# Kernel tuning notes

Measured on AMD Instinct MI355X. Metric: run time of the kernel, lower is better.

## Reference

```python
import jax, jax.numpy as jnp
import numpy as np

N_T = 100  # number of time grid points for the ODE solve, matching torch.linspace(0, 1, 100)


def setup_inputs() -> dict:
    key = jax.random.key(0)
    kx, kw, kb, kc, kd = jax.random.split(key, 5)
    H = 1024
    N = 16384
    return {
        "x": jax.random.normal(kx, (N, H), dtype=jnp.float32),
        "W": jax.random.normal(kw, (H, H), dtype=jnp.float32),
        "b": jax.random.normal(kb, (H,), dtype=jnp.float32),
        "c": jax.random.normal(kc, (H,), dtype=jnp.float32),
        "d": jax.random.normal(kd, (H,), dtype=jnp.float32),
    }


def reference(x, W, b, c, d):
    # fused matmul + trig elementwise: z = x @ W + b*sin(x) + c*cos(x) + d*tan(x)
    z = jnp.matmul(x, W) + b * jnp.sin(x) + c * jnp.cos(x) + d * jnp.tan(x)

    # ODE: dy/dt = -y + t*z, y(0)=0, integrated on linspace(0,1,100), return y(1).
    ts = jnp.linspace(0.0, 1.0, N_T, dtype=z.dtype)
    t0 = ts[:-1]
    dts = ts[1:] - ts[:-1]

    def f(t, y):
        return -y + t * z

    def rk4_step(y, t_dt):
        t, dt = t_dt
        k1 = f(t, y)
        k2 = f(t + 0.5 * dt, y + 0.5 * dt * k1)
        k3 = f(t + 0.5 * dt, y + 0.5 * dt * k2)
        k4 = f(t + dt, y + dt * k3)
        y_next = y + (dt / 6.0) * (k1 + 2.0 * k2 + 2.0 * k3 + k4)
        return y_next, None

    y0 = jnp.zeros_like(z)
    y_final, _ = jax.lax.scan(rk4_step, y0, (t0, dts))
    return y_final
```

## Files before the change

### kernel.cpp

```cpp
#include <hip/hip_runtime.h>
#include <hip/hip_bf16.h>

typedef __attribute__((ext_vector_type(4))) float  f32x4;
typedef __attribute__((ext_vector_type(8))) short  bf16x8;
typedef __attribute__((ext_vector_type(4))) short  bf16x4v;

#define BM 128
#define BN 128
#define BK 64
#define PADK 72
#define EPAD 68
#define SMEM_BYTES 36864

__device__ __forceinline__ unsigned short f2bf(float f) {
  __hip_bfloat16 h = __float2bfloat16(f);
  unsigned short u; __builtin_memcpy(&u, &h, 2); return u;
}
__device__ __forceinline__ float bf2f(short u) {
  unsigned int w = ((unsigned int)(unsigned short)u) << 16;
  float f; __builtin_memcpy(&f, &w, 4); return f;
}

__device__ __forceinline__ void my_sincos(float xf, float& s_out, float& c_out) {
  const float kf = __builtin_rintf(xf * 0.636619772367581343f);
  const int   q  = (int)kf;
  const double kd = (double)kf;
  double rd = __builtin_fma(-kd, 1.5707963267948966,    (double)xf);
  rd        = __builtin_fma(-kd, 6.123233995736766e-17, rd);
  const float r = (float)rd;
  const float z = r * r;
  const float ps = fmaf(z, fmaf(z, fmaf(z, 2.7183114939898219e-06f,
                                           -1.9839334836096632e-04f),
                                   8.3333293858894632e-03f),
                        -1.6666666641626524e-01f);
  const float sr = fmaf(r * z, ps, r);
  const float pc = fmaf(z, fmaf(z, fmaf(z, 2.4390448796277409e-05f,
                                           -1.3886763774609929e-03f),
                                   4.1666623323739063e-02f),
                        -4.9999999725103100e-01f);
  const float cr = fmaf(z, pc, 1.0f);
  const bool swap = (q & 1) != 0;
  float s1 = swap ? cr : sr;
  float c1 = swap ? sr : cr;
  if (q & 2)       s1 = -s1;
  if ((q + 1) & 2) c1 = -c1;
  s_out = s1; c_out = c1;
}

__global__ __launch_bounds__(256)
void prep_all(const float* __restrict__ W, const float* __restrict__ x,
              const float* __restrict__ bv, const float* __restrict__ cv,
              const float* __restrict__ dv,
              unsigned short* __restrict__ Wt, unsigned short* __restrict__ xb,
              unsigned short* __restrict__ g, int H, int n4) {
  __shared__ float tile[64][65];
  const int t = threadIdx.x;
  if (blockIdx.x < 256) {
    const int blk = blockIdx.x;
    const int n0 = (blk & 15) << 6;
    const int k0 = (blk >> 4) << 6;
    #pragma unroll
    for (int it = 0; it < 4; ++it) {
      int q = it * 256 + t;
      int r = q >> 4, c4 = (q & 15) << 2;
      f32x4 v = *(const f32x4*)&W[(size_t)(k0 + r) * H + n0 + c4];
      tile[r][c4 + 0] = v[0]; tile[r][c4 + 1] = v[1];
      tile[r][c4 + 2] = v[2]; tile[r][c4 + 3] = v[3];
    }
    __syncthreads();
    #pragma unroll
    for (int it = 0; it < 4; ++it) {
      int q = it * 256 + t;
      int r = q >> 4, c4 = (q & 15) << 2;
      bf16x4v o;
      #pragma unroll
      for (int j = 0; j < 4; ++j) o[j] = (short)f2bf(tile[c4 + j][r]);
      *(bf16x4v*)&Wt[(size_t)(n0 + r) * H + k0 + c4] = o;
    }
  } else {
    const int jm = (H >> 2) - 1;
    int i = (blockIdx.x - 256) * 256 + t;
    const int stride = ((int)gridDim.x - 256) * 256;
    for (; i < n4; i += stride) {
      f32x4 v = ((const f32x4*)x)[i];
      const int j4 = (i & jm) << 2;
      f32x4 b4 = *(const f32x4*)&bv[j4];
      f32x4 c4 = *(const f32x4*)&cv[j4];
      f32x4 d4 = *(const f32x4*)&dv[j4];
      bf16x4v xo, go;
      #pragma unroll
      for (int e = 0; e < 4; ++e) {
        xo[e] = (short)f2bf(v[e]);
        float s, co;
        my_sincos(v[e], s, co);
        const float tn = s * __builtin_amdgcn_rcpf(co);
        go[e] = (short)f2bf(fmaf(b4[e], s, fmaf(c4[e], co, d4[e] * tn)));
      }
      ((bf16x4v*)xb)[i] = xo;
      ((bf16x4v*)g)[i]  = go;
    }
  }
}

__global__ __launch_bounds__(256)
void transpose_W(const float* __restrict__ W, unsigned short* __restrict__ Wt, int H) {
  __shared__ float tile[64][65];
  const int k0 = blockIdx.y * 64;
  const int n0 = blockIdx.x * 64;
  const int t = threadIdx.x;
  #pragma unroll
  for (int it = 0; it < 4; ++it) {
    int q = it * 256 + t;
    int r = q >> 4, c4 = (q & 15) << 2;
    f32x4 v = *(const f32x4*)&W[(size_t)(k0 + r) * H + n0 + c4];
    tile[r][c4 + 0] = v[0]; tile[r][c4 + 1] = v[1];
    tile[r][c4 + 2] = v[2]; tile[r][c4 + 3] = v[3];
  }
  __syncthreads();
  #pragma unroll
  for (int it = 0; it < 4; ++it) {
    int q = it * 256 + t;
    int r = q >> 4, c4 = (q & 15) << 2;
    bf16x4v o;
    #pragma unroll
    for (int j = 0; j < 4; ++j) o[j] = (short)f2bf(tile[c4 + j][r]);
    *(bf16x4v*)&Wt[(size_t)(n0 + r) * H + k0 + c4] = o;
  }
}
__global__ __launch_bounds__(256)
void cvt_x(const float* __restrict__ x, unsigned short* __restrict__ xb, int n4) {
  int i = blockIdx.x * 256 + threadIdx.x;
  const int stride = gridDim.x * 256;
  for (; i < n4; i += stride) {
    f32x4 v = ((const f32x4*)x)[i];
    bf16x4v o;
    #pragma unroll
    for (int j = 0; j < 4; ++j) o[j] = (short)f2bf(v[j]);
    ((bf16x4v*)xb)[i] = o;
  }
}

template <int MODE>
__global__ __launch_bounds__(256, 2)
void gemm_fused(const float* __restrict__ x, const unsigned short* __restrict__ xb,
                const unsigned short* __restrict__ Wt,
                const unsigned short* __restrict__ g,
                const float* __restrict__ bv, const float* __restrict__ cv,
                const float* __restrict__ dv, float* __restrict__ out,
                float S, int H) {
  __shared__ unsigned char smem[SMEM_BYTES];
  unsigned short* As = (unsigned short*)smem;
  unsigned short* Bs = As + BM * PADK;
  float*          Es = (float*)smem;

  const int tid  = threadIdx.x;
  const int nwg  = gridDim.x;
  const int work = (blockIdx.x & 7) * (nwg >> 3) + (blockIdx.x >> 3);
  const int bj   = work & 7;
  const int bi   = work >> 3;
  const int i0   = bi * BM, j0 = bj * BN;
  const int wave = tid >> 6, lane = tid & 63;
  const int wr = wave >> 1, wc = wave & 1;
  const int l16 = lane & 15, lq = lane >> 4;

  f32x4 acc[4][4] = {};

  for (int kk = 0; kk < H; kk += BK) {
    if constexpr (MODE <= 1) {
      #pragma unroll
      for (int it = 0; it < 4; ++it) {
        int q = it * 256 + tid;
        int r = q >> 3, c8 = (q & 7) << 3;
        bf16x8 v = *(const bf16x8*)&xb[(size_t)(i0 + r) * H + kk + c8];
        *(bf16x8*)&As[r * PADK + c8] = v;
      }
    } else {
      #pragma unroll
      for (int it = 0; it < 8; ++it) {
        int q = it * 256 + tid;
        int r = q >> 4, c4 = (q & 15) << 2;
        f32x4 v = *(const f32x4*)&x[(size_t)(i0 + r) * H + kk + c4];
        bf16x4v o;
        #pragma unroll
        for (int j = 0; j < 4; ++j) o[j] = (short)f2bf(v[j]);
        *(bf16x4v*)&As[r * PADK + c4] = o;
      }
    }
    #pragma unroll
    for (int it = 0; it < 4; ++it) {
      int q = it * 256 + tid;
      int r = q >> 3, c8 = (q & 7) << 3;
      bf16x8 v = *(const bf16x8*)&Wt[(size_t)(j0 + r) * H + kk + c8];
      *(bf16x8*)&Bs[r * PADK + c8] = v;
    }
    __syncthreads();

    #pragma unroll
    for (int s = 0; s < 2; ++s) {
      bf16x8 af[4], bfr[4];
      #pragma unroll
      for (int mi = 0; mi < 4; ++mi)
        af[mi] = *(const bf16x8*)&As[(wr * 64 + mi * 16 + l16) * PADK + s * 32 + lq * 8];
      #pragma unroll
      for (int ni = 0; ni < 4; ++ni)
        bfr[ni] = *(const bf16x8*)&Bs[(wc * 64 + ni * 16 + l16) * PADK + s * 32 + lq * 8];
      #pragma unroll
      for (int mi = 0; mi < 4; ++mi)
        #pragma unroll
        for (int ni = 0; ni < 4; ++ni)
          acc[mi][ni] = __builtin_amdgcn_mfma_f32_16x16x32_bf16(af[mi], bfr[ni], acc[mi][ni], 0, 0, 0);
    }
    __syncthreads();
  }

  float* ep = Es + wave * (16 * EPAD);
  const int rr = lane >> 2;
  const int cq = (lane & 3) * 16;
  #pragma unroll
  for (int mi = 0; mi < 4; ++mi) {
    #pragma unroll
    for (int ni = 0; ni < 4; ++ni)
      #pragma unroll
      for (int r = 0; r < 4; ++r)
        ep[(lq * 4 + r) * EPAD + ni * 16 + l16] = acc[mi][ni][r];
    const int i  = i0 + wr * 64 + mi * 16 + rr;
    const int jb = j0 + wc * 64 + cq;
    float* orow = &out[(size_t)i * H + jb];
    if constexpr (MODE == 0) {
      const unsigned short* grow = &g[(size_t)i * H + jb];
      #pragma unroll
      for (int t = 0; t < 4; ++t) {
        f32x4 a = *(const f32x4*)&ep[rr * EPAD + cq + 4 * t];
        bf16x4v gv = *(const bf16x4v*)&grow[4 * t];
        f32x4 o;
        #pragma unroll
        for (int e = 0; e < 4; ++e) o[e] = S * (a[e] + bf2f(gv[e]));
        *(f32x4*)&orow[4 * t] = o;
      }
    } else {
      const float* xrow = &x[(size_t)i * H + jb];
      #pragma unroll
      for (int t = 0; t < 4; ++t) {
        f32x4 a  = *(const f32x4*)&ep[rr * EPAD + cq + 4 * t];
        f32x4 xv = *(const f32x4*)&xrow[4 * t];
        f32x4 b4 = *(const f32x4*)&bv[jb + 4 * t];
        f32x4 c4 = *(const f32x4*)&cv[jb + 4 * t];
        f32x4 d4 = *(const f32x4*)&dv[jb + 4 * t];
        f32x4 o;
        #pragma unroll
        for (int e = 0; e < 4; ++e) {
          float s, co;
          my_sincos(xv[e], s, co);
          const float tanv = s * __builtin_amdgcn_rcpf(co);
          o[e] = S * (fmaf(b4[e], s, a[e]) + fmaf(c4[e], co, d4[e] * tanv));
        }
        *(f32x4*)&orow[4 * t] = o;
      }
    }
  }
}

extern "C" void kernel_launch(void* const* d_in, const int* in_sizes, int n_in,
                              void* d_out, int out_size, void* d_ws, size_t ws_size,
                              hipStream_t stream) {
  const float* x = (const float*)d_in[0];
  const float* W = (const float*)d_in[1];
  const float* b = (const float*)d_in[2];
  const float* c = (const float*)d_in[3];
  const float* d = (const float*)d_in[4];
  float* out = (float*)d_out;
  const int H = in_sizes[2];
  const int M = in_sizes[0] / H;

  const int NT = 100;
  float ts[NT];
  const float step = (float)(1.0 / 99.0);
  for (int i = 0; i < NT; ++i) ts[i] = (float)i * step;
  ts[NT - 1] = 1.0f;
  double yy = 0.0;
  for (int i = 0; i < NT - 1; ++i) {
    const double t = (double)ts[i], dt = (double)(ts[i + 1] - ts[i]);
    const double k1 = t - yy;
    const double k2 = (t + 0.5 * dt) - (yy + 0.5 * dt * k1);
    const double k3 = (t + 0.5 * dt) - (yy + 0.5 * dt * k2);
    const double k4 = (t + dt) - (yy + dt * k3);
    yy += dt / 6.0 * (k1 + 2.0 * k2 + 2.0 * k3 + k4);
  }
  const float S = (float)yy;

  unsigned short* Wt = (unsigned short*)d_ws;
  unsigned short* xb = Wt + (size_t)H * H;
  unsigned short* g  = xb + (size_t)M * H;
  const size_t needW  = (size_t)H * H * 2;
  const size_t needXb = (size_t)M * H * 2;
  const int n4   = M * H / 4;
  const int nblk = (H / BN) * (M / BM);

  if (ws_size >= needW + 2 * needXb) {
    prep_all<<<256 + 2048, 256, 0, stream>>>(W, x, b, c, d, Wt, xb, g, H, n4);
    gemm_fused<0><<<nblk, 256, 0, stream>>>(x, xb, Wt, g, b, c, d, out, S, H);
  } else if (ws_size >= needW + needXb) {
    dim3 tgrid(H / 64, H / 64);
    transpose_W<<<tgrid, 256, 0, stream>>>(W, Wt, H);
    cvt_x<<<2048, 256, 0, stream>>>(x, xb, n4);
    gemm_fused<1><<<nblk, 256, 0, stream>>>(x, xb, Wt, nullptr, b, c, d, out, S, H);
  } else {
    dim3 tgrid(H / 64, H / 64);
    transpose_W<<<tgrid, 256, 0, stream>>>(W, Wt, H);
    gemm_fused<2><<<nblk, 256, 0, stream>>>(x, nullptr, Wt, nullptr, b, c, d, out, S, H);
  }
}
```

Measured before the change: 85.92 us.

## Double-buffer GEMM K-loop with direct global-to-LDS loads in MODE 0

For MODE 0, the GEMM main loop now uses __builtin_amdgcn_global_load_lds to stream bf16 A and B tiles straight into LDS. The tiles are double-buffered with BK=32 so the next tile's load overlaps the current MFMA work, and there is one barrier per step. This removes the register round-trip for tile staging and the second barrier per iteration. The tiles use an unpadded 32-element row layout, which risks LDS bank conflicts on fragment reads. Launch bounds are also raised to 4 blocks per CU to allow higher occupancy, at the cost of register pressure.

```diff
diff --git a/kernel.cpp b/kernel.cpp
--- a/kernel.cpp
+++ b/kernel.cpp
@@ -7,7 +7,6 @@
 
 #define BM 128
 #define BN 128
-#define BK 64
 #define PADK 72
 #define EPAD 68
 #define SMEM_BYTES 36864
@@ -141,7 +140,7 @@
 }
 
 template <int MODE>
-__global__ __launch_bounds__(256, 2)
+__global__ __launch_bounds__(256, 4)
 void gemm_fused(const float* __restrict__ x, const unsigned short* __restrict__ xb,
                 const unsigned short* __restrict__ Wt,
                 const unsigned short* __restrict__ g,
@@ -149,9 +148,7 @@
                 const float* __restrict__ dv, float* __restrict__ out,
                 float S, int H) {
   __shared__ unsigned char smem[SMEM_BYTES];
-  unsigned short* As = (unsigned short*)smem;
-  unsigned short* Bs = As + BM * PADK;
-  float*          Es = (float*)smem;
+  float* Es = (float*)smem;
 
   const int tid  = threadIdx.x;
   const int nwg  = gridDim.x;
@@ -165,52 +162,103 @@
 
   f32x4 acc[4][4] = {};
 
-  for (int kk = 0; kk < H; kk += BK) {
-    if constexpr (MODE <= 1) {
+  if constexpr (MODE == 0) {
+    const int sRow = wave * 32 + (lane >> 2);
+    const int sCol = (lane & 3) << 3;
+    const unsigned short* aS0 = &xb[(size_t)(i0 + sRow)      * H + sCol];
+    const unsigned short* aS1 = &xb[(size_t)(i0 + sRow + 16) * H + sCol];
+    const unsigned short* bS0 = &Wt[(size_t)(j0 + sRow)      * H + sCol];
+    const unsigned short* bS1 = &Wt[(size_t)(j0 + sRow + 16) * H + sCol];
+    const int ldsOff = wave * 2048;
+
+    #define STAGE(bufsel, kOff)                                                      \
+      do {                                                                           \
+        char* _b = (char*)smem + (bufsel) * 16384 + ldsOff;                          \
+        __builtin_amdgcn_global_load_lds(                                            \
+          (const __attribute__((address_space(1))) void*)(aS0 + (kOff)),             \
+          (__attribute__((address_space(3))) void*)(_b), 16, 0, 0);                  \
+        __builtin_amdgcn_global_load_lds(                                            \
+          (const __attribute__((address_space(1))) void*)(aS1 + (kOff)),             \
+          (__attribute__((address_space(3))) void*)(_b + 1024), 16, 0, 0);           \
+        __builtin_amdgcn_global_load_lds(                                            \
+          (const __attribute__((address_space(1))) void*)(bS0 + (kOff)),             \
+          (__attribute__((address_space(3))) void*)(_b + 8192), 16, 0, 0);           \
+        __builtin_amdgcn_global_load_lds(                                            \
+          (const __attribute__((address_space(1))) void*)(bS1 + (kOff)),             \
+          (__attribute__((address_space(3))) void*)(_b + 8192 + 1024), 16, 0, 0);    \
+      } while (0)
+
+    const int nsteps = H >> 5;
+    STAGE(0, 0);
+    __syncthreads();
+    for (int t = 0; t < nsteps; ++t) {
+      if (t + 1 < nsteps) STAGE((t + 1) & 1, (t + 1) * 32);
+      const unsigned short* Ab = (const unsigned short*)(smem + (t & 1) * 16384);
+      const unsigned short* Bb = Ab + 8192 / 2;
+      bf16x8 af[4], bfr[4];
+      #pragma unroll
+      for (int mi = 0; mi < 4; ++mi)
+        af[mi] = *(const bf16x8*)&Ab[(wr * 64 + mi * 16 + l16) * 32 + lq * 8];
+      #pragma unroll
+      for (int ni = 0; ni < 4; ++ni)
+        bfr[ni] = *(const bf16x8*)&Bb[(wc * 64 + ni * 16 + l16) * 32 + lq * 8];
+      #pragma unroll
+      for (int mi = 0; mi < 4; ++mi)
+        #pragma unroll
+        for (int ni = 0; ni < 4; ++ni)
+          acc[mi][ni] = __builtin_amdgcn_mfma_f32_16x16x32_bf16(af[mi], bfr[ni], acc[mi][ni], 0, 0, 0);
+      __syncthreads();
+    }
+    #undef STAGE
+  } else {
+    unsigned short* As = (unsigned short*)smem;
+    unsigned short* Bs = As + BM * PADK;
+    for (int kk = 0; kk < H; kk += 64) {
+      if constexpr (MODE == 1) {
+        #pragma unroll
+        for (int it = 0; it < 4; ++it) {
+          int q = it * 256 + tid;
+          int r = q >> 3, c8 = (q & 7) << 3;
+          bf16x8 v = *(const bf16x8*)&xb[(size_t)(i0 + r) * H + kk + c8];
+          *(bf16x8*)&As[r * PADK + c8] = v;
+        }
+      } else {
+        #pragma unroll
+        for (int it = 0; it < 8; ++it) {
+          int q = it * 256 + tid;
+          int r = q >> 4, c4 = (q & 15) << 2;
+          f32x4 v = *(const f32x4*)&x[(size_t)(i0 + r) * H + kk + c4];
+          bf16x4v o;
+          #pragma unroll
+          for (int j = 0; j < 4; ++j) o[j] = (short)f2bf(v[j]);
+          *(bf16x4v*)&As[r * PADK + c4] = o;
+        }
+      }
       #pragma unroll
       for (int it = 0; it < 4; ++it) {
         int q = it * 256 + tid;
         int r = q >> 3, c8 = (q & 7) << 3;
-        bf16x8 v = *(const bf16x8*)&xb[(size_t)(i0 + r) * H + kk + c8];
-        *(bf16x8*)&As[r * PADK + c8] = v;
-      }
-    } else {
-      #pragma unroll
-      for (int it = 0; it < 8; ++it) {
-        int q = it * 256 + tid;
-        int r = q >> 4, c4 = (q & 15) << 2;
-        f32x4 v = *(const f32x4*)&x[(size_t)(i0 + r) * H + kk + c4];
-        bf16x4v o;
-        #pragma unroll
-        for (int j = 0; j < 4; ++j) o[j] = (short)f2bf(v[j]);
-        *(bf16x4v*)&As[r * PADK + c4] = o;
-      }
-    }
-    #pragma unroll
-    for (int it = 0; it < 4; ++it) {
-      int q = it * 256 + tid;
-      int r = q >> 3, c8 = (q & 7) << 3;
-      bf16x8 v = *(const bf16x8*)&Wt[(size_t)(j0 + r) * H + kk + c8];
-      *(bf16x8*)&Bs[r * PADK + c8] = v;
-    }
-    __syncthreads();
-
-    #pragma unroll
-    for (int s = 0; s < 2; ++s) {
-      bf16x8 af[4], bfr[4];
-      #pragma unroll
-      for (int mi = 0; mi < 4; ++mi)
-        af[mi] = *(const bf16x8*)&As[(wr * 64 + mi * 16 + l16) * PADK + s * 32 + lq * 8];
-      #pragma unroll
-      for (int ni = 0; ni < 4; ++ni)
-        bfr[ni] = *(const bf16x8*)&Bs[(wc * 64 + ni * 16 + l16) * PADK + s * 32 + lq * 8];
-      #pragma unroll
-      for (int mi = 0; mi < 4; ++mi)
+        bf16x8 v = *(const bf16x8*)&Wt[(size_t)(j0 + r) * H + kk + c8];
+        *(bf16x8*)&Bs[r * PADK + c8] = v;
+      }
+      __syncthreads();
+      #pragma unroll
+      for (int s = 0; s < 2; ++s) {
+        bf16x8 af[4], bfr[4];
+        #pragma unroll
+        for (int mi = 0; mi < 4; ++mi)
+          af[mi] = *(const bf16x8*)&As[(wr * 64 + mi * 16 + l16) * PADK + s * 32 + lq * 8];
         #pragma unroll
         for (int ni = 0; ni < 4; ++ni)
-          acc[mi][ni] = __builtin_amdgcn_mfma_f32_16x16x32_bf16(af[mi], bfr[ni], acc[mi][ni], 0, 0, 0);
-    }
-    __syncthreads();
+          bfr[ni] = *(const bf16x8*)&Bs[(wc * 64 + ni * 16 + l16) * PADK + s * 32 + lq * 8];
+        #pragma unroll
+        for (int mi = 0; mi < 4; ++mi)
+          #pragma unroll
+          for (int ni = 0; ni < 4; ++ni)
+            acc[mi][ni] = __builtin_amdgcn_mfma_f32_16x16x32_bf16(af[mi], bfr[ni], acc[mi][ni], 0, 0, 0);
+      }
+      __syncthreads();
+    }
   }
 
   float* ep = Es + wave * (16 * EPAD);
```

After: 86.53 us. Within noise of the previous version (+0.7%).

## Pipeline GEMM mainloop with direct global-to-LDS loads and triple buffering

Applied to the files above, without the earlier changes.

For the MODE 0 path, the GEMM mainloop now issues global_load_lds loads straight into LDS using a swizzled layout, across three 16KB buffers with BK=32. A manual vmcnt wait and a single barrier per step replace the load-to-register, store-to-LDS and double-__syncthreads pattern, so memory fetches overlap MFMA work. Occupancy is raised to 3 blocks per CU and MFMA issue priority is boosted with s_setprio. The larger shared memory footprint and tighter register budget could limit occupancy or cause spills, and the hand-counted vmcnt values must match the number of loads in flight.

```diff
diff --git a/kernel.cpp b/kernel.cpp
--- a/kernel.cpp
+++ b/kernel.cpp
@@ -7,10 +7,11 @@
 
 #define BM 128
 #define BN 128
-#define BK 64
 #define PADK 72
 #define EPAD 68
-#define SMEM_BYTES 36864
+#define SMEM_BYTES 49152
+#define AS1 __attribute__((address_space(1)))
+#define AS3 __attribute__((address_space(3)))
 
 __device__ __forceinline__ unsigned short f2bf(float f) {
   __hip_bfloat16 h = __float2bfloat16(f);
@@ -141,7 +142,7 @@
 }
 
 template <int MODE>
-__global__ __launch_bounds__(256, 2)
+__global__ __launch_bounds__(256, 3)
 void gemm_fused(const float* __restrict__ x, const unsigned short* __restrict__ xb,
                 const unsigned short* __restrict__ Wt,
                 const unsigned short* __restrict__ g,
@@ -149,9 +150,7 @@
                 const float* __restrict__ dv, float* __restrict__ out,
                 float S, int H) {
   __shared__ unsigned char smem[SMEM_BYTES];
-  unsigned short* As = (unsigned short*)smem;
-  unsigned short* Bs = As + BM * PADK;
-  float*          Es = (float*)smem;
+  float* Es = (float*)smem;
 
   const int tid  = threadIdx.x;
   const int nwg  = gridDim.x;
@@ -165,52 +164,121 @@
 
   f32x4 acc[4][4] = {};
 
-  for (int kk = 0; kk < H; kk += BK) {
-    if constexpr (MODE <= 1) {
+  if constexpr (MODE == 0) {
+    const int halfA = wr * 4096;
+    const int halfB = 8192 + wc * 4096;
+    const unsigned short* aP[4];
+    const unsigned short* bP[4];
+    #pragma unroll
+    for (int k = 0; k < 4; ++k) {
+      const int D   = k * 1024 + lane * 16;
+      const int sup = D >> 7;
+      const int sl  = ((D >> 4) & 7) ^ (sup & 7);
+      const int r   = sup * 2 + (sl >> 2);
+      const int c   = (sl & 3) << 3;
+      aP[k] = &xb[(size_t)(i0 + wr * 64 + r) * H + c];
+      bP[k] = &Wt[(size_t)(j0 + wc * 64 + r) * H + c];
+    }
+
+    #define STAGE(tt)                                                                \
+      do {                                                                           \
+        char* _buf = (char*)smem + ((tt) % 3) * 16384;                               \
+        const int _k = (tt) << 5;                                                    \
+        _Pragma("unroll")                                                            \
+        for (int k = 0; k < 4; ++k) {                                                \
+          __builtin_amdgcn_global_load_lds(                                          \
+            (const AS1 void*)(aP[k] + _k),                                           \
+            (AS3 void*)(_buf + halfA + k * 1024), 16, 0, 0);                         \
+          __builtin_amdgcn_global_load_lds(                                          \
+            (const AS1 void*)(bP[k] + _k),                                           \
+            (AS3 void*)(_buf + halfB + k * 1024), 16, 0, 0);                         \
+        }                                                                            \
+      } while (0)
+
+    int aOff[4], bOff[4];
+    #pragma unroll
+    for (int m = 0; m < 4; ++m) {
+      const int R = m * 16 + l16;
+      const int o = (R >> 1) * 128 + ((4 * (R & 1) + lq) ^ ((R >> 1) & 7)) * 16;
+      aOff[m] = o; bOff[m] = o;
+    }
+
+    const int nsteps = H >> 5;
+    STAGE(0);
+    STAGE(1);
+    for (int t = 0; t < nsteps; ++t) {
+      if (t + 2 < nsteps) STAGE(t + 2);
+      if (t < nsteps - 2)       asm volatile("s_waitcnt vmcnt(16)" ::: "memory");
+      else if (t == nsteps - 2) asm volatile("s_waitcnt vmcnt(8)"  ::: "memory");
+      else                      asm volatile("s_waitcnt vmcnt(0)"  ::: "memory");
+      const char* buf = (const char*)smem + (t % 3) * 16384;
+      const char* Ah = buf + halfA;
+      const char* Bh = buf + halfB;
+      bf16x8 af[4], bfr[4];
+      #pragma unroll
+      for (int mi = 0; mi < 4; ++mi) af[mi]  = *(const bf16x8*)(Ah + aOff[mi]);
+      #pragma unroll
+      for (int ni = 0; ni < 4; ++ni) bfr[ni] = *(const bf16x8*)(Bh + bOff[ni]);
+      __builtin_amdgcn_s_setprio(1);
+      #pragma unroll
+      for (int mi = 0; mi < 4; ++mi)
+        #pragma unroll
+        for (int ni = 0; ni < 4; ++ni)
+          acc[mi][ni] = __builtin_amdgcn_mfma_f32_16x16x32_bf16(af[mi], bfr[ni], acc[mi][ni], 0, 0, 0);
+      __builtin_amdgcn_s_setprio(0);
+      __builtin_amdgcn_s_barrier();
+    }
+    #undef STAGE
+    __syncthreads();
+  } else {
+    unsigned short* As = (unsigned short*)smem;
+    unsigned short* Bs = As + BM * PADK;
+    for (int kk = 0; kk < H; kk += 64) {
+      if constexpr (MODE == 1) {
+        #pragma unroll
+        for (int it = 0; it < 4; ++it) {
+          int q = it * 256 + tid;
+          int r = q >> 3, c8 = (q & 7) << 3;
+          bf16x8 v = *(const bf16x8*)&xb[(size_t)(i0 + r) * H + kk + c8];
+          *(bf16x8*)&As[r * PADK + c8] = v;
+        }
+      } else {
+        #pragma unroll
+        for (int it = 0; it < 8; ++it) {
+          int q = it * 256 + tid;
+          int r = q >> 4, c4 = (q & 15) << 2;
+          f32x4 v = *(const f32x4*)&x[(size_t)(i0 + r) * H + kk + c4];
+          bf16x4v o;
+          #pragma unroll
+          for (int j = 0; j < 4; ++j) o[j] = (short)f2bf(v[j]);
+          *(bf16x4v*)&As[r * PADK + c4] = o;
+        }
+      }
       #pragma unroll
       for (int it = 0; it < 4; ++it) {
         int q = it * 256 + tid;
         int r = q >> 3, c8 = (q & 7) << 3;
-        bf16x8 v = *(const bf16x8*)&xb[(size_t)(i0 + r) * H + kk + c8];
-        *(bf16x8*)&As[r * PADK + c8] = v;
-      }
-    } else {
-      #pragma unroll
-      for (int it = 0; it < 8; ++it) {
-        int q = it * 256 + tid;
-        int r = q >> 4, c4 = (q & 15) << 2;
-        f32x4 v = *(const f32x4*)&x[(size_t)(i0 + r) * H + kk + c4];
-        bf16x4v o;
-        #pragma unroll
-        for (int j = 0; j < 4; ++j) o[j] = (short)f2bf(v[j]);
-        *(bf16x4v*)&As[r * PADK + c4] = o;
-      }
-    }
-    #pragma unroll
-    for (int it = 0; it < 4; ++it) {
-      int q = it * 256 + tid;
-      int r = q >> 3, c8 = (q & 7) << 3;
-      bf16x8 v = *(const bf16x8*)&Wt[(size_t)(j0 + r) * H + kk + c8];
-      *(bf16x8*)&Bs[r * PADK + c8] = v;
-    }
-    __syncthreads();
-
-    #pragma unroll
-    for (int s = 0; s < 2; ++s) {
-      bf16x8 af[4], bfr[4];
-      #pragma unroll
-      for (int mi = 0; mi < 4; ++mi)
-        af[mi] = *(const bf16x8*)&As[(wr * 64 + mi * 16 + l16) * PADK + s * 32 + lq * 8];
-      #pragma unroll
-      for (int ni = 0; ni < 4; ++ni)
-        bfr[ni] = *(const bf16x8*)&Bs[(wc * 64 + ni * 16 + l16) * PADK + s * 32 + lq * 8];
-      #pragma unroll
-      for (int mi = 0; mi < 4; ++mi)
+        bf16x8 v = *(const bf16x8*)&Wt[(size_t)(j0 + r) * H + kk + c8];
+        *(bf16x8*)&Bs[r * PADK + c8] = v;
+      }
+      __syncthreads();
+      #pragma unroll
+      for (int s = 0; s < 2; ++s) {
+        bf16x8 af[4], bfr[4];
+        #pragma unroll
+        for (int mi = 0; mi < 4; ++mi)
+          af[mi] = *(const bf16x8*)&As[(wr * 64 + mi * 16 + l16) * PADK + s * 32 + lq * 8];
         #pragma unroll
         for (int ni = 0; ni < 4; ++ni)
-          acc[mi][ni] = __builtin_amdgcn_mfma_f32_16x16x32_bf16(af[mi], bfr[ni], acc[mi][ni], 0, 0, 0);
-    }
-    __syncthreads();
+          bfr[ni] = *(const bf16x8*)&Bs[(wc * 64 + ni * 16 + l16) * PADK + s * 32 + lq * 8];
+        #pragma unroll
+        for (int mi = 0; mi < 4; ++mi)
+          #pragma unroll
+          for (int ni = 0; ni < 4; ++ni)
+            acc[mi][ni] = __builtin_amdgcn_mfma_f32_16x16x32_bf16(af[mi], bfr[ni], acc[mi][ni], 0, 0, 0);
+      }
+      __syncthreads();
+    }
   }
 
   float* ep = Es + wave * (16 * EPAD);
```

Result: slower. 94.49 us (+10.0%).

## Keep W column block resident in LDS and stream A directly from global

Applied to the files above, without the earlier changes.

Replaces the main 128x128 tiled GEMM with a 256x64 tile kernel (512 threads). Each half of the 64-column W slice (64x512 bf16) is staged into LDS through async global_load_lds with an XOR swizzle. A fragments are read directly from global memory into registers instead of going through LDS. This cuts LDS traffic for A and the per-k-step barriers, at the cost of uncached-by-LDS A reads, more loads of A per output column block, and a shape-restricted fast path.

```diff
diff --git a/kernel.cpp b/kernel.cpp
--- a/kernel.cpp
+++ b/kernel.cpp
@@ -5,12 +5,9 @@
 typedef __attribute__((ext_vector_type(8))) short  bf16x8;
 typedef __attribute__((ext_vector_type(4))) short  bf16x4v;
 
-#define BM 128
-#define BN 128
-#define BK 64
-#define PADK 72
 #define EPAD 68
-#define SMEM_BYTES 36864
+#define AS1 __attribute__((address_space(1)))
+#define AS3 __attribute__((address_space(3)))
 
 __device__ __forceinline__ unsigned short f2bf(float f) {
   __hip_bfloat16 h = __float2bfloat16(f);
@@ -140,39 +137,142 @@
   }
 }
 
-template <int MODE>
-__global__ __launch_bounds__(256, 2)
-void gemm_fused(const float* __restrict__ x, const unsigned short* __restrict__ xb,
-                const unsigned short* __restrict__ Wt,
-                const unsigned short* __restrict__ g,
-                const float* __restrict__ bv, const float* __restrict__ cv,
-                const float* __restrict__ dv, float* __restrict__ out,
-                float S, int H) {
-  __shared__ unsigned char smem[SMEM_BYTES];
-  unsigned short* As = (unsigned short*)smem;
-  unsigned short* Bs = As + BM * PADK;
-  float*          Es = (float*)smem;
+__global__ __launch_bounds__(512, 4)
+void gemm_wres(const unsigned short* __restrict__ xb,
+               const unsigned short* __restrict__ Wt,
+               const unsigned short* __restrict__ g,
+               float* __restrict__ out, float S, int H) {
+  __shared__ unsigned char smem[65536];
+  float* Es = (float*)smem;
 
   const int tid  = threadIdx.x;
   const int nwg  = gridDim.x;
   const int work = (blockIdx.x & 7) * (nwg >> 3) + (blockIdx.x >> 3);
-  const int bj   = work & 7;
-  const int bi   = work >> 3;
-  const int i0   = bi * BM, j0 = bj * BN;
+  const int bj   = work & 15;
+  const int bi   = work >> 4;
+  const int i0   = bi * 256, j0 = bj * 64;
+  const int wave = tid >> 6, lane = tid & 63;
+  const int l16  = lane & 15, lq = lane >> 4;
+
+  const int t8    = tid & 255;
+  const int sup   = t8 >> 3;
+  const int slotL = (t8 & 7) ^ (sup & 7);
+  const int srow  = sup * 2 + (slotL >> 2);
+  const int scol  = (slotL & 3) << 3;
+  const unsigned short* sP = &Wt[(size_t)(j0 + srow) * H + (tid >> 8) * 32 + scol];
+
+  #define STAGEH(h)                                                            \
+    do {                                                                       \
+      _Pragma("unroll")                                                        \
+      for (int is = 0; is < 8; ++is)                                           \
+        __builtin_amdgcn_global_load_lds(                                      \
+          (const AS1 void*)(sP + (h) * 512 + is * 64),                         \
+          (AS3 void*)((char*)smem + is * 8192 + tid * 16), 16, 0, 0);          \
+    } while (0)
+
+  int bOff[4];
+  #pragma unroll
+  for (int ni = 0; ni < 4; ++ni) {
+    const int R = ni * 16 + l16;
+    bOff[ni] = (R >> 1) * 128 + ((4 * (R & 1) + lq) ^ ((R >> 1) & 7)) * 16;
+  }
+  const unsigned short* aB0 = &xb[(size_t)(i0 + wave * 32 +  0 + l16) * H + lq * 8];
+  const unsigned short* aB1 = &xb[(size_t)(i0 + wave * 32 + 16 + l16) * H + lq * 8];
+
+  f32x4 acc[2][4] = {};
+
+  STAGEH(0);
+  __syncthreads();
+  #pragma unroll 4
+  for (int kt = 0; kt < 16; ++kt) {
+    const int ko = kt * 32;
+    bf16x8 a0 = *(const bf16x8*)(aB0 + ko);
+    bf16x8 a1 = *(const bf16x8*)(aB1 + ko);
+    const char* tb = (const char*)smem + kt * 4096;
+    #pragma unroll
+    for (int ni = 0; ni < 4; ++ni) {
+      bf16x8 bf = *(const bf16x8*)(tb + bOff[ni]);
+      acc[0][ni] = __builtin_amdgcn_mfma_f32_16x16x32_bf16(a0, bf, acc[0][ni], 0, 0, 0);
+      acc[1][ni] = __builtin_amdgcn_mfma_f32_16x16x32_bf16(a1, bf, acc[1][ni], 0, 0, 0);
+    }
+  }
+  __syncthreads();
+  STAGEH(1);
+  __syncthreads();
+  #pragma unroll 4
+  for (int kt = 0; kt < 16; ++kt) {
+    const int ko = 512 + kt * 32;
+    bf16x8 a0 = *(const bf16x8*)(aB0 + ko);
+    bf16x8 a1 = *(const bf16x8*)(aB1 + ko);
+    const char* tb = (const char*)smem + kt * 4096;
+    #pragma unroll
+    for (int ni = 0; ni < 4; ++ni) {
+      bf16x8 bf = *(const bf16x8*)(tb + bOff[ni]);
+      acc[0][ni] = __builtin_amdgcn_mfma_f32_16x16x32_bf16(a0, bf, acc[0][ni], 0, 0, 0);
+      acc[1][ni] = __builtin_amdgcn_mfma_f32_16x16x32_bf16(a1, bf, acc[1][ni], 0, 0, 0);
+    }
+  }
+  __syncthreads();
+  #undef STAGEH
+
+  float* ep = Es + wave * (16 * EPAD);
+  const int rr = lane >> 2;
+  const int cq = (lane & 3) * 16;
+  #pragma unroll
+  for (int mi = 0; mi < 2; ++mi) {
+    #pragma unroll
+    for (int ni = 0; ni < 4; ++ni)
+      #pragma unroll
+      for (int r = 0; r < 4; ++r)
+        ep[(lq * 4 + r) * EPAD + ni * 16 + l16] = acc[mi][ni][r];
+    const int i  = i0 + wave * 32 + mi * 16 + rr;
+    const int jb = j0 + cq;
+    float* orow = &out[(size_t)i * H + jb];
+    const unsigned short* grow = &g[(size_t)i * H + jb];
+    #pragma unroll
+    for (int t = 0; t < 4; ++t) {
+      f32x4 a = *(const f32x4*)&ep[rr * EPAD + cq + 4 * t];
+      bf16x4v gv = *(const bf16x4v*)&grow[4 * t];
+      f32x4 o;
+      #pragma unroll
+      for (int e = 0; e < 4; ++e) o[e] = S * (a[e] + bf2f(gv[e]));
+      *(f32x4*)&orow[4 * t] = o;
+    }
+  }
+}
+
+template <int MODE>
+__global__ __launch_bounds__(256, 2)
+void gemm_fb(const float* __restrict__ x, const unsigned short* __restrict__ xb,
+             const unsigned short* __restrict__ Wt,
+             const float* __restrict__ bv, const float* __restrict__ cv,
+             const float* __restrict__ dv, float* __restrict__ out,
+             float S, int H) {
+  __shared__ unsigned char smem[36864];
+  unsigned short* As = (unsigned short*)smem;
+  unsigned short* Bs = As + 128 * 72;
+  float*          Es = (float*)smem;
+
+  const int tid  = threadIdx.x;
+  const int nwg  = gridDim.x;
+  const int work = (nwg % 8 == 0) ? (blockIdx.x & 7) * (nwg >> 3) + (blockIdx.x >> 3)
+                                  : blockIdx.x;
+  const int nbj  = H / 128;
+  const int bj   = work % nbj;
+  const int bi   = work / nbj;
+  const int i0   = bi * 128, j0 = bj * 128;
   const int wave = tid >> 6, lane = tid & 63;
   const int wr = wave >> 1, wc = wave & 1;
   const int l16 = lane & 15, lq = lane >> 4;
 
   f32x4 acc[4][4] = {};
-
-  for (int kk = 0; kk < H; kk += BK) {
-    if constexpr (MODE <= 1) {
+  for (int kk = 0; kk < H; kk += 64) {
+    if constexpr (MODE == 1) {
       #pragma unroll
       for (int it = 0; it < 4; ++it) {
         int q = it * 256 + tid;
         int r = q >> 3, c8 = (q & 7) << 3;
-        bf16x8 v = *(const bf16x8*)&xb[(size_t)(i0 + r) * H + kk + c8];
-        *(bf16x8*)&As[r * PADK + c8] = v;
+        *(bf16x8*)&As[r * 72 + c8] = *(const bf16x8*)&xb[(size_t)(i0 + r) * H + kk + c8];
       }
     } else {
       #pragma unroll
@@ -183,27 +283,25 @@
         bf16x4v o;
         #pragma unroll
         for (int j = 0; j < 4; ++j) o[j] = (short)f2bf(v[j]);
-        *(bf16x4v*)&As[r * PADK + c4] = o;
+        *(bf16x4v*)&As[r * 72 + c4] = o;
       }
     }
     #pragma unroll
     for (int it = 0; it < 4; ++it) {
       int q = it * 256 + tid;
       int r = q >> 3, c8 = (q & 7) << 3;
-      bf16x8 v = *(const bf16x8*)&Wt[(size_t)(j0 + r) * H + kk + c8];
-      *(bf16x8*)&Bs[r * PADK + c8] = v;
+      *(bf16x8*)&Bs[r * 72 + c8] = *(const bf16x8*)&Wt[(size_t)(j0 + r) * H + kk + c8];
     }
     __syncthreads();
-
     #pragma unroll
     for (int s = 0; s < 2; ++s) {
       bf16x8 af[4], bfr[4];
       #pragma unroll
       for (int mi = 0; mi < 4; ++mi)
-        af[mi] = *(const bf16x8*)&As[(wr * 64 + mi * 16 + l16) * PADK + s * 32 + lq * 8];
+        af[mi] = *(const bf16x8*)&As[(wr * 64 + mi * 16 + l16) * 72 + s * 32 + lq * 8];
       #pragma unroll
       for (int ni = 0; ni < 4; ++ni)
-        bfr[ni] = *(const bf16x8*)&Bs[(wc * 64 + ni * 16 + l16) * PADK + s * 32 + lq * 8];
+        bfr[ni] = *(const bf16x8*)&Bs[(wc * 64 + ni * 16 + l16) * 72 + s * 32 + lq * 8];
       #pragma unroll
       for (int mi = 0; mi < 4; ++mi)
         #pragma unroll
@@ -212,7 +310,6 @@
     }
     __syncthreads();
   }
-
   float* ep = Es + wave * (16 * EPAD);
   const int rr = lane >> 2;
   const int cq = (lane & 3) * 16;
@@ -225,37 +322,24 @@
         ep[(lq * 4 + r) * EPAD + ni * 16 + l16] = acc[mi][ni][r];
     const int i  = i0 + wr * 64 + mi * 16 + rr;
     const int jb = j0 + wc * 64 + cq;
-    float* orow = &out[(size_t)i * H + jb];
-    if constexpr (MODE == 0) {
-      const unsigned short* grow = &g[(size_t)i * H + jb];
-      #pragma unroll
-      for (int t = 0; t < 4; ++t) {
-        f32x4 a = *(const f32x4*)&ep[rr * EPAD + cq + 4 * t];
-        bf16x4v gv = *(const bf16x4v*)&grow[4 * t];
-        f32x4 o;
-        #pragma unroll
-        for (int e = 0; e < 4; ++e) o[e] = S * (a[e] + bf2f(gv[e]));
-        *(f32x4*)&orow[4 * t] = o;
+    const float* xrow = &x[(size_t)i * H + jb];
+    float*       orow = &out[(size_t)i * H + jb];
+    #pragma unroll
+    for (int t = 0; t < 4; ++t) {
+      f32x4 a  = *(const f32x4*)&ep[rr * EPAD + cq + 4 * t];
+      f32x4 xv = *(const f32x4*)&xrow[4 * t];
+      f32x4 b4 = *(const f32x4*)&bv[jb + 4 * t];
+      f32x4 c4 = *(const f32x4*)&cv[jb + 4 * t];
+      f32x4 d4 = *(const f32x4*)&dv[jb + 4 * t];
+      f32x4 o;
+      #pragma unroll
+      for (int e = 0; e < 4; ++e) {
+        float s, co;
+        my_sincos(xv[e], s, co);
+        const float tanv = s * __builtin_amdgcn_rcpf(co);
+        o[e] = S * (fmaf(b4[e], s, a[e]) + fmaf(c4[e], co, d4[e] * tanv));
       }
-    } else {
-      const float* xrow = &x[(size_t)i * H + jb];
-      #pragma unroll
-      for (int t = 0; t < 4; ++t) {
-        f32x4 a  = *(const f32x4*)&ep[rr * EPAD + cq + 4 * t];
-        f32x4 xv = *(const f32x4*)&xrow[4 * t];
-        f32x4 b4 = *(const f32x4*)&bv[jb + 4 * t];
-        f32x4 c4 = *(const f32x4*)&cv[jb + 4 * t];
-        f32x4 d4 = *(const f32x4*)&dv[jb + 4 * t];
-        f32x4 o;
-        #pragma unroll
-        for (int e = 0; e < 4; ++e) {
-          float s, co;
-          my_sincos(xv[e], s, co);
-          const float tanv = s * __builtin_amdgcn_rcpf(co);
-          o[e] = S * (fmaf(b4[e], s, a[e]) + fmaf(c4[e], co, d4[e] * tanv));
-        }
-        *(f32x4*)&orow[4 * t] = o;
-      }
+      *(f32x4*)&orow[4 * t] = o;
     }
   }
 }
@@ -293,20 +377,22 @@
   unsigned short* g  = xb + (size_t)M * H;
   const size_t needW  = (size_t)H * H * 2;
   const size_t needXb = (size_t)M * H * 2;
-  const int n4   = M * H / 4;
-  const int nblk = (H / BN) * (M / BM);
-
-  if (ws_size >= needW + 2 * needXb) {
+  const int n4 = M * H / 4;
+
+  const bool shapeOK = (H == 1024) && (M % 256 == 0) && ((M / 256) * 16 % 8 == 0);
+
+  if (ws_size >= needW + 2 * needXb && shapeOK) {
     prep_all<<<256 + 2048, 256, 0, stream>>>(W, x, b, c, d, Wt, xb, g, H, n4);
-    gemm_fused<0><<<nblk, 256, 0, stream>>>(x, xb, Wt, g, b, c, d, out, S, H);
+    const int nblk = (M / 256) * 16;
+    gemm_wres<<<nblk, 512, 0, stream>>>(xb, Wt, g, out, S, H);
   } else if (ws_size >= needW + needXb) {
     dim3 tgrid(H / 64, H / 64);
     transpose_W<<<tgrid, 256, 0, stream>>>(W, Wt, H);
     cvt_x<<<2048, 256, 0, stream>>>(x, xb, n4);
-    gemm_fused<1><<<nblk, 256, 0, stream>>>(x, xb, Wt, nullptr, b, c, d, out, S, H);
+    gemm_fb<1><<<(H / 128) * (M / 128), 256, 0, stream>>>(x, xb, Wt, b, c, d, out, S, H);
   } else {
     dim3 tgrid(H / 64, H / 64);
     transpose_W<<<tgrid, 256, 0, stream>>>(W, Wt, H);
-    gemm_fused<2><<<nblk, 256, 0, stream>>>(x, nullptr, Wt, nullptr, b, c, d, out, S, H);
-  }
-}
+    gemm_fb<2><<<(H / 128) * (M / 128), 256, 0, stream>>>(x, nullptr, Wt, b, c, d, out, S, H);
+  }
+}
```

Result: slower. 112.9 us (+31.4%).
